# Kernel optimization log

Hardware: AMD Instinct MI355X
Metric: run time of the kernel (lower is better)

## Reference

```python
import jax, jax.numpy as jnp
import numpy as np

N = 100000      # nodes
E = 1600000     # edges (avg degree 16)
IN = 512        # input feature dim
H, C = 8, 8     # conv1: 8 heads x 8 channels (hardcoded in module)
HID = H * C     # 64
OUT = 64        # output classes (conv2: 1 head, no concat)
NEG_SLOPE = 0.2 # PyG GATConv default leaky-relu slope


def setup_inputs() -> dict:
    key = jax.random.key(0)
    ks = jax.random.split(key, 10)
    x = jax.random.normal(ks[0], (N, IN), dtype=jnp.float32)
    edge_index = jax.random.randint(ks[1], (2, E), 0, N, dtype=jnp.int32)
    W1 = jax.random.normal(ks[2], (IN, HID), dtype=jnp.float32) / np.sqrt(IN).astype(np.float32)
    a_src1 = jax.random.normal(ks[3], (H, C), dtype=jnp.float32) * 0.1
    a_dst1 = jax.random.normal(ks[4], (H, C), dtype=jnp.float32) * 0.1
    b1 = jnp.zeros((HID,), dtype=jnp.float32)
    W2 = jax.random.normal(ks[5], (HID, OUT), dtype=jnp.float32) / np.sqrt(HID).astype(np.float32)
    a_src2 = jax.random.normal(ks[6], (1, OUT), dtype=jnp.float32) * 0.1
    a_dst2 = jax.random.normal(ks[7], (1, OUT), dtype=jnp.float32) * 0.1
    b2 = jnp.zeros((OUT,), dtype=jnp.float32)
    return {"x": x, "edge_index": edge_index, "W1": W1, "a_src1": a_src1,
            "a_dst1": a_dst1, "b1": b1, "W2": W2, "a_src2": a_src2,
            "a_dst2": a_dst2, "b2": b2}


def _gat_attend(h, src, dst, a_s, a_d, n_nodes):
    """h: [N,H,C]; src/dst: [E]; a_s/a_d: [H,C] -> aggregated [N,H,C]."""
    # per-node half-scores (PyG decomposition of a^T [Wx_i || Wx_j])
    sc_s = jnp.sum(h * a_s, axis=-1)                       # [N,H]
    sc_d = jnp.sum(h * a_d, axis=-1)                       # [N,H]
    logits = jax.nn.leaky_relu(sc_s[src] + sc_d[dst], NEG_SLOPE)  # [E,H]
    # segment softmax over edges grouped by destination node
    mx = jax.ops.segment_max(logits, dst, num_segments=n_nodes)   # [N,H]
    ex = jnp.exp(logits - mx[dst])                          # [E,H]
    denom = jax.ops.segment_sum(ex, dst, num_segments=n_nodes)    # [N,H]
    alpha = ex / (denom[dst] + 1e-16)                       # [E,H]
    msg = h[src] * alpha[:, :, None]                        # [E,H,C]
    return jax.ops.segment_sum(msg, dst, num_segments=n_nodes)    # [N,H,C]


def reference(x, edge_index, W1, a_src1, a_dst1, b1, W2, a_src2, a_dst2, b2):
    n = x.shape[0]
    loop = jnp.arange(n, dtype=edge_index.dtype)
    src = jnp.concatenate([edge_index[0], loop])            # self-loops (PyG default)
    dst = jnp.concatenate([edge_index[1], loop])
    # conv1: 8 heads, concat
    h1 = (x @ W1).reshape(n, H, C)
    o1 = _gat_attend(h1, src, dst, a_src1, a_dst1, n).reshape(n, HID) + b1
    x2 = jax.nn.elu(o1)
    # conv2: 1 head, no concat
    h2 = (x2 @ W2).reshape(n, 1, OUT)
    o2 = _gat_attend(h2, src, dst, a_src2, a_dst2, n)[:, 0] + b2
    return jax.nn.log_softmax(o2, axis=1)
```

## Files before the change

kernel.cpp:

```cpp
#include <hip/hip_runtime.h>
#include <cstdint>
#include <cstddef>

#define LEAKY 0.2f
#define NEG_INF -3.402823466e38f
static const int CHUNK = 2048;

typedef __attribute__((ext_vector_type(8))) short short8;
typedef __attribute__((ext_vector_type(4))) float floatx4;

__device__ __forceinline__ float dot4(float4 a, float4 b) {
    return a.x * b.x + a.y * b.y + a.z * b.z + a.w * b.w;
}

__device__ __forceinline__ unsigned short f2bf(float f) {
    unsigned u = __float_as_uint(f);
    u += 0x7fffu + ((u >> 16) & 1u);
    return (unsigned short)(u >> 16);
}
__device__ __forceinline__ float bf2f(unsigned short u) {
    return __uint_as_float(((unsigned)u) << 16);
}
__device__ __forceinline__ float bflo(unsigned u) { return __uint_as_float(u << 16); }
__device__ __forceinline__ float bfhi(unsigned u) { return __uint_as_float(u & 0xffff0000u); }

__global__ __launch_bounds__(256) void k_init_deg(int* __restrict__ deg, int Nn) {
    int i = blockIdx.x * 256 + threadIdx.x;
    if (i < Nn) deg[i] = 1;
}

__global__ __launch_bounds__(256) void k_count_p(const int* __restrict__ ei, int* __restrict__ deg,
                                                 int E, int Nn) {
    int part = blockIdx.x & 7;
    int lo = (int)((long long)Nn * part >> 3);
    int hi = (int)((long long)Nn * (part + 1) >> 3);
    int nthr = (gridDim.x >> 3) * 256;
    int tid = (blockIdx.x >> 3) * 256 + threadIdx.x;
    for (int e = tid; e < E; e += nthr) {
        int d = ei[E + e];
        if (d >= lo && d < hi) atomicAdd(&deg[d], 1);
    }
}

__global__ __launch_bounds__(256) void k_scan1(const int* __restrict__ deg, int* __restrict__ bsum, int Nn) {
    __shared__ int sm[256];
    int b = blockIdx.x, t = threadIdx.x;
    int s = 0;
    int i0 = b * CHUNK + t * 8;
#pragma unroll
    for (int j = 0; j < 8; ++j) { int i = i0 + j; if (i < Nn) s += deg[i]; }
    sm[t] = s;
    __syncthreads();
    for (int o = 128; o; o >>= 1) { if (t < o) sm[t] += sm[t + o]; __syncthreads(); }
    if (t == 0) bsum[b] = sm[0];
}

__global__ __launch_bounds__(256) void k_scan3(const int* __restrict__ deg, const int* __restrict__ bsum,
                                               int* __restrict__ indptr, int* __restrict__ cursor,
                                               int Nn, int B) {
    __shared__ int wsum[4];
    int b = blockIdx.x, t = threadIdx.x, lane = t & 63, w = t >> 6;

    int vb = (lane < B) ? bsum[lane] : 0;
    int incb = vb;
#pragma unroll
    for (int o = 1; o < 64; o <<= 1) { int u = __shfl_up(incb, o); if (lane >= o) incb += u; }
    int bpre_b = __shfl(incb - vb, b);

    int i0 = b * CHUNK + t * 8;
    int d[8]; int s = 0;
#pragma unroll
    for (int j = 0; j < 8; ++j) { int i = i0 + j; d[j] = (i < Nn) ? deg[i] : 0; s += d[j]; }
    int inc = s;
#pragma unroll
    for (int o = 1; o < 64; o <<= 1) { int u = __shfl_up(inc, o); if (lane >= o) inc += u; }
    if (lane == 63) wsum[w] = inc;
    __syncthreads();
    int wofs = 0;
    for (int k = 0; k < w; ++k) wofs += wsum[k];
    int base = bpre_b + wofs + (inc - s);
    int run = 0;
#pragma unroll
    for (int j = 0; j < 8; ++j) {
        int i = i0 + j;
        if (i < Nn) {
            int v = base + run;
            indptr[i] = v; cursor[i] = v;
            run += d[j];
            if (i == Nn - 1) indptr[Nn] = v + d[j];
        }
    }
}

__global__ __launch_bounds__(256) void k_fill_p(const int* __restrict__ ei, int* __restrict__ cursor,
                                                int* __restrict__ csr, int E, int Nn) {
    int part = blockIdx.x & 7;
    int lo = (int)((long long)Nn * part >> 3);
    int hi = (int)((long long)Nn * (part + 1) >> 3);
    int nthr = (gridDim.x >> 3) * 256;
    int tid = (blockIdx.x >> 3) * 256 + threadIdx.x;
    int tot = E + Nn;
    for (int idx = tid; idx < tot; idx += nthr) {
        int d = (idx < E) ? ei[E + idx] : idx - E;
        if (d >= lo && d < hi) {
            int s = (idx < E) ? ei[idx] : idx - E;
            int slot = atomicAdd(&cursor[d], 1);
            csr[slot] = s;
        }
    }
}

__global__ __launch_bounds__(256) void k_prepW(const float* __restrict__ W1, unsigned short* __restrict__ W1t) {
    int i = blockIdx.x * 256 + threadIdx.x;
    if (i >= 64 * 512) return;
    int n = i >> 9, k = i & 511;
    W1t[i] = f2bf(W1[k * 64 + n]);
}

__global__ __launch_bounds__(256) void gemm1_mfma(const float* __restrict__ A, const unsigned short* __restrict__ W1t,
                                                  unsigned short* __restrict__ C, int M) {
    __shared__ __align__(16) unsigned short As[128][40];
    __shared__ __align__(16) unsigned short Bs[64][40];
    int t = threadIdx.x;
    int w = t >> 6, l = t & 63;
    int quad = l >> 4, lm = l & 15;
    int row0 = blockIdx.x * 128;

    floatx4 acc[2][4] = {};

    for (int k0 = 0; k0 < 512; k0 += 32) {
#pragma unroll
        for (int j = 0; j < 4; ++j) {
            int f = t + 256 * j;
            int r = f >> 3, c4 = f & 7;
            int rg = row0 + r; if (rg >= M) rg = M - 1;
            float4 v = *(const float4*)(A + (size_t)rg * 512 + k0 + c4 * 4);
            ushort4 b; b.x = f2bf(v.x); b.y = f2bf(v.y); b.z = f2bf(v.z); b.w = f2bf(v.w);
            *(ushort4*)&As[r][c4 * 4] = b;
        }
        {
            int n = t >> 2, seg = t & 3;
            *(uint4*)&Bs[n][seg * 8] = *(const uint4*)(W1t + (size_t)n * 512 + k0 + seg * 8);
        }
        __syncthreads();

        short8 af[2], bfm[4];
#pragma unroll
        for (int tm = 0; tm < 2; ++tm) {
            int m = w * 32 + tm * 16 + lm;
            af[tm] = *(const short8*)&As[m][quad * 8];
        }
#pragma unroll
        for (int tn = 0; tn < 4; ++tn) {
            int n = tn * 16 + lm;
            bfm[tn] = *(const short8*)&Bs[n][quad * 8];
        }
#pragma unroll
        for (int tm = 0; tm < 2; ++tm)
#pragma unroll
            for (int tn = 0; tn < 4; ++tn)
                acc[tm][tn] = __builtin_amdgcn_mfma_f32_16x16x32_bf16(af[tm], bfm[tn], acc[tm][tn], 0, 0, 0);
        __syncthreads();
    }

#pragma unroll
    for (int tm = 0; tm < 2; ++tm) {
#pragma unroll
        for (int r = 0; r < 4; ++r) {
            int row = row0 + w * 32 + tm * 16 + quad * 4 + r;
            if (row < M) {
#pragma unroll
                for (int tn = 0; tn < 4; ++tn)
                    C[(size_t)row * 64 + tn * 16 + lm] = f2bf(acc[tm][tn][r]);
            }
        }
    }
}

template <int KB>
__global__ __launch_bounds__(256) void gemm_n64(const float* __restrict__ A, const float* __restrict__ B,
                                                unsigned short* __restrict__ C, int M, int K) {
    __shared__ float As[KB][68];
    __shared__ float Bs[KB][68];
    int tid = threadIdx.x;
    int row0 = blockIdx.x * 64;
    int tx = tid & 15, ty = tid >> 4;
    float acc[4][4] = {};
    for (int k0 = 0; k0 < K; k0 += KB) {
#pragma unroll
        for (int j = 0; j < (64 * KB) / (256 * 4); ++j) {
            int f = tid + 256 * j;
            int r = f / (KB / 4);
            int c4 = f % (KB / 4);
            int rg = row0 + r; if (rg >= M) rg = M - 1;
            float4 v = *(const float4*)(A + (size_t)rg * K + k0 + c4 * 4);
            As[c4 * 4 + 0][r] = v.x; As[c4 * 4 + 1][r] = v.y;
            As[c4 * 4 + 2][r] = v.z; As[c4 * 4 + 3][r] = v.w;
        }
#pragma unroll
        for (int j = 0; j < (KB * 64) / (256 * 4); ++j) {
            int f = tid + 256 * j;
            int kk = f / 16, c4 = f % 16;
            *(float4*)&Bs[kk][c4 * 4] = *(const float4*)(B + (size_t)(k0 + kk) * 64 + c4 * 4);
        }
        __syncthreads();
#pragma unroll
        for (int kk = 0; kk < KB; ++kk) {
            float4 a = *(const float4*)&As[kk][ty * 4];
            float4 b = *(const float4*)&Bs[kk][tx * 4];
            float av[4] = {a.x, a.y, a.z, a.w};
            float bv[4] = {b.x, b.y, b.z, b.w};
#pragma unroll
            for (int i = 0; i < 4; ++i)
#pragma unroll
                for (int j = 0; j < 4; ++j) acc[i][j] += av[i] * bv[j];
        }
        __syncthreads();
    }
#pragma unroll
    for (int i = 0; i < 4; ++i) {
        int rg = row0 + ty * 4 + i;
        if (rg < M) {
            ushort4 b; b.x = f2bf(acc[i][0]); b.y = f2bf(acc[i][1]);
            b.z = f2bf(acc[i][2]); b.w = f2bf(acc[i][3]);
            *(ushort4*)(C + (size_t)rg * 64 + tx * 4) = b;
        }
    }
}

__global__ __launch_bounds__(256) void k_sc1(const unsigned short* __restrict__ h1, const float* __restrict__ as1,
                                             const float* __restrict__ ad1, float* __restrict__ scs,
                                             float* __restrict__ scd, int Nn) {
    int i = blockIdx.x * 256 + threadIdx.x;
    if (i >= Nn * 8) return;
    int h = i & 7;
    ushort4 p0 = *(const ushort4*)(h1 + (size_t)i * 8);
    ushort4 p1 = *(const ushort4*)(h1 + (size_t)i * 8 + 4);
    float4 v0 = make_float4(bf2f(p0.x), bf2f(p0.y), bf2f(p0.z), bf2f(p0.w));
    float4 v1 = make_float4(bf2f(p1.x), bf2f(p1.y), bf2f(p1.z), bf2f(p1.w));
    const float4* asp = (const float4*)(as1 + h * 8);
    const float4* adp = (const float4*)(ad1 + h * 8);
    scs[i] = dot4(v0, asp[0]) + dot4(v1, asp[1]);
    scd[i] = dot4(v0, adp[0]) + dot4(v1, adp[1]);
}

__global__ __launch_bounds__(256) void k_sc2(const unsigned short* __restrict__ h2, const float* __restrict__ as2,
                                             const float* __restrict__ ad2, float* __restrict__ scs,
                                             float* __restrict__ scd, int Nn) {
    int wave = (blockIdx.x * 256 + threadIdx.x) >> 6;
    int lane = threadIdx.x & 63;
    if (wave >= Nn) return;
    float v = bf2f(h2[(size_t)wave * 64 + lane]);
    float ss = v * as2[lane], sd = v * ad2[lane];
#pragma unroll
    for (int o = 32; o; o >>= 1) { ss += __shfl_xor(ss, o); sd += __shfl_xor(sd, o); }
    if (lane == 0) { scs[wave] = ss; scd[wave] = sd; }
}

__global__ __launch_bounds__(256) void k_agg1(const unsigned short* __restrict__ h1, const float* __restrict__ scs,
                                              const float* __restrict__ scd, const int* __restrict__ indptr,
                                              const int* __restrict__ csr, const float* __restrict__ b1,
                                              float* __restrict__ x2, int Nn) {
    int node = (blockIdx.x * 256 + threadIdx.x) >> 6;
    int l = threadIdx.x & 63;
    if (node >= Nn) return;
    int h8 = l & 7, grp = l >> 3;
    int start = indptr[node], end = indptr[node + 1];
    float sd = scd[node * 8 + h8];

    float dsum = 0.f;
    float acc8[8] = {};
    for (int base = start; base < end; base += 64) {
        int e = base + l;
        int s64 = csr[e < end ? e : start];
        int cnt = min(64, end - base);
        int nb = (cnt + 7) >> 3;
#pragma unroll
        for (int b = 0; b < 8; ++b) {
            if (b < nb) {
                int slot = base + b * 8 + grp;
                int sb = __shfl(s64, b * 8 + grp);
                float v = scs[sb * 8 + h8] + sd;
                v = v > 0.f ? v : LEAKY * v;
                float ex = (slot < end) ? __expf(v) : 0.f;
                dsum += ex;
                uint4 q = *(const uint4*)(h1 + (size_t)sb * 64 + h8 * 8);
                acc8[0] += ex * bflo(q.x); acc8[1] += ex * bfhi(q.x);
                acc8[2] += ex * bflo(q.y); acc8[3] += ex * bfhi(q.y);
                acc8[4] += ex * bflo(q.z); acc8[5] += ex * bfhi(q.z);
                acc8[6] += ex * bflo(q.w); acc8[7] += ex * bfhi(q.w);
            }
        }
    }
#pragma unroll
    for (int o = 8; o < 64; o <<= 1) {
        dsum += __shfl_xor(dsum, o);
#pragma unroll
        for (int k = 0; k < 8; ++k) acc8[k] += __shfl_xor(acc8[k], o);
    }
    if (grp == 0) {
        float inv = 1.f / (dsum + 1e-16f);
        float4 ba = *((const float4*)b1 + h8 * 2);
        float4 bb = *((const float4*)b1 + h8 * 2 + 1);
        float o0 = acc8[0] * inv + ba.x, o1 = acc8[1] * inv + ba.y;
        float o2 = acc8[2] * inv + ba.z, o3 = acc8[3] * inv + ba.w;
        float o4 = acc8[4] * inv + bb.x, o5 = acc8[5] * inv + bb.y;
        float o6 = acc8[6] * inv + bb.z, o7 = acc8[7] * inv + bb.w;
        o0 = o0 > 0.f ? o0 : expm1f(o0); o1 = o1 > 0.f ? o1 : expm1f(o1);
        o2 = o2 > 0.f ? o2 : expm1f(o2); o3 = o3 > 0.f ? o3 : expm1f(o3);
        o4 = o4 > 0.f ? o4 : expm1f(o4); o5 = o5 > 0.f ? o5 : expm1f(o5);
        o6 = o6 > 0.f ? o6 : expm1f(o6); o7 = o7 > 0.f ? o7 : expm1f(o7);
        float* dst = x2 + (size_t)node * 64 + h8 * 8;
        *(float4*)dst = make_float4(o0, o1, o2, o3);
        *(float4*)(dst + 4) = make_float4(o4, o5, o6, o7);
    }
}

__global__ __launch_bounds__(256) void k_agg2(const unsigned short* __restrict__ h2, const float* __restrict__ scs,
                                              const float* __restrict__ scd, const int* __restrict__ indptr,
                                              const int* __restrict__ csr, const float* __restrict__ b2,
                                              float* __restrict__ out, int Nn) {
    int node = (blockIdx.x * 256 + threadIdx.x) >> 6;
    int l = threadIdx.x & 63;
    if (node >= Nn) return;
    int g = l >> 3, c8 = l & 7;
    int start = indptr[node], end = indptr[node + 1];
    float sd = scd[node];

    float dsum = 0.f;
    float acc8[8] = {};
    for (int base = start; base < end; base += 64) {
        int e = base + l;
        int s64 = csr[e < end ? e : start];
        float v = scs[s64] + sd;
        v = v > 0.f ? v : LEAKY * v;
        float ex = (e < end) ? __expf(v) : 0.f;
        dsum += ex;
        int cnt = min(64, end - base);
        int nb = (cnt + 7) >> 3;
#pragma unroll 2
        for (int b = 0; b < nb; ++b) {
            float exv = __shfl(ex, b * 8 + g);
            int sb = __shfl(s64, b * 8 + g);
            uint4 q = *(const uint4*)(h2 + (size_t)sb * 64 + c8 * 8);
            acc8[0] += exv * bflo(q.x); acc8[1] += exv * bfhi(q.x);
            acc8[2] += exv * bflo(q.y); acc8[3] += exv * bfhi(q.y);
            acc8[4] += exv * bflo(q.z); acc8[5] += exv * bfhi(q.z);
            acc8[6] += exv * bflo(q.w); acc8[7] += exv * bfhi(q.w);
        }
    }
#pragma unroll
    for (int o = 32; o; o >>= 1) dsum += __shfl_xor(dsum, o);
#pragma unroll
    for (int o = 8; o < 64; o <<= 1)
#pragma unroll
        for (int k = 0; k < 8; ++k) acc8[k] += __shfl_xor(acc8[k], o);

    float inv = 1.f / (dsum + 1e-16f);
    float4 ba = *((const float4*)b2 + c8 * 2);
    float4 bb = *((const float4*)b2 + c8 * 2 + 1);
    float ov[8];
    ov[0] = acc8[0] * inv + ba.x; ov[1] = acc8[1] * inv + ba.y;
    ov[2] = acc8[2] * inv + ba.z; ov[3] = acc8[3] * inv + ba.w;
    ov[4] = acc8[4] * inv + bb.x; ov[5] = acc8[5] * inv + bb.y;
    ov[6] = acc8[6] * inv + bb.z; ov[7] = acc8[7] * inv + bb.w;

    float m2 = ov[0];
#pragma unroll
    for (int k = 1; k < 8; ++k) m2 = fmaxf(m2, ov[k]);
#pragma unroll
    for (int o = 1; o < 8; o <<= 1) m2 = fmaxf(m2, __shfl_xor(m2, o));
    float se = 0.f;
#pragma unroll
    for (int k = 0; k < 8; ++k) se += __expf(ov[k] - m2);
#pragma unroll
    for (int o = 1; o < 8; o <<= 1) se += __shfl_xor(se, o);
    float ls = m2 + __logf(se);
    if (g == 0) {
        float* dst = out + (size_t)node * 64 + c8 * 8;
        *(float4*)dst = make_float4(ov[0] - ls, ov[1] - ls, ov[2] - ls, ov[3] - ls);
        *(float4*)(dst + 4) = make_float4(ov[4] - ls, ov[5] - ls, ov[6] - ls, ov[7] - ls);
    }
}

extern "C" void kernel_launch(void* const* d_in, const int* in_sizes, int n_in,
                              void* d_out, int out_size, void* d_ws, size_t ws_size,
                              hipStream_t stream) {
    (void)n_in; (void)out_size; (void)ws_size;
    const float* x   = (const float*)d_in[0];
    const int*   ei  = (const int*)d_in[1];
    const float* W1  = (const float*)d_in[2];
    const float* as1 = (const float*)d_in[3];
    const float* ad1 = (const float*)d_in[4];
    const float* b1  = (const float*)d_in[5];
    const float* W2  = (const float*)d_in[6];
    const float* as2 = (const float*)d_in[7];
    const float* ad2 = (const float*)d_in[8];
    const float* b2  = (const float*)d_in[9];
    float* out = (float*)d_out;

    const int N = in_sizes[0] / 512;
    const int E = in_sizes[1] / 2;

    char* p = (char*)d_ws;
    auto alloc = [&](size_t bytes) -> char* {
        char* r = p; p += (bytes + 255) & ~(size_t)255; return r;
    };
    unsigned short* h1bf = (unsigned short*)alloc((size_t)N * 64 * 2);
    float* x2    = (float*)alloc((size_t)N * 64 * 4);
    unsigned short* h2bf = h1bf;
    float* sc1s  = (float*)alloc((size_t)N * 8 * 4);
    float* sc1d  = (float*)alloc((size_t)N * 8 * 4);
    float* sc2s  = (float*)alloc((size_t)N * 4);
    float* sc2d  = (float*)alloc((size_t)N * 4);
    int*   deg   = (int*)alloc((size_t)N * 4);
    int*   cursor= (int*)alloc((size_t)N * 4);
    int*   indptr= (int*)alloc((size_t)(N + 1) * 4);
    int*   csr   = (int*)alloc((size_t)(E + N) * 4);
    int*   bsum  = (int*)alloc(64 * 4);
    unsigned short* W1t = (unsigned short*)alloc(64 * 512 * 2);

    const int B = (N + CHUNK - 1) / CHUNK;

    k_init_deg<<<(N + 255) / 256, 256, 0, stream>>>(deg, N);
    k_count_p<<<1024, 256, 0, stream>>>(ei, deg, E, N);
    k_scan1  <<<B, 256, 0, stream>>>(deg, bsum, N);
    k_scan3  <<<B, 256, 0, stream>>>(deg, bsum, indptr, cursor, N, B);
    k_fill_p <<<1024, 256, 0, stream>>>(ei, cursor, csr, E, N);

    k_prepW<<<(64 * 512 + 255) / 256, 256, 0, stream>>>(W1, W1t);
    gemm1_mfma<<<(N + 127) / 128, 256, 0, stream>>>(x, W1t, h1bf, N);
    k_sc1 <<<(N * 8 + 255) / 256, 256, 0, stream>>>(h1bf, as1, ad1, sc1s, sc1d, N);
    k_agg1<<<(N + 3) / 4, 256, 0, stream>>>(h1bf, sc1s, sc1d, indptr, csr, b1, x2, N);

    gemm_n64<64><<<(N + 63) / 64, 256, 0, stream>>>(x2, W2, h2bf, N, 64);
    k_sc2 <<<(N + 3) / 4, 256, 0, stream>>>(h2bf, as2, ad2, sc2s, sc2d, N);
    k_agg2<<<(N + 3) / 4, 256, 0, stream>>>(h2bf, sc2s, sc2d, indptr, csr, b2, out, N);
}
```

Before: 629.8 us.

## Fuse attention score computation into GEMM epilogues and batch gather loads in aggregation

```diff
diff --git a/kernel.cpp b/kernel.cpp
--- a/kernel.cpp
+++ b/kernel.cpp
@@ -24,8 +24,13 @@
 __device__ __forceinline__ float bflo(unsigned u) { return __uint_as_float(u << 16); }
 __device__ __forceinline__ float bfhi(unsigned u) { return __uint_as_float(u & 0xffff0000u); }
 
-__global__ __launch_bounds__(256) void k_init_deg(int* __restrict__ deg, int Nn) {
+__global__ __launch_bounds__(256) void k_misc(const float* __restrict__ W1, unsigned short* __restrict__ W1t,
+                                              int* __restrict__ deg, int Nn) {
     int i = blockIdx.x * 256 + threadIdx.x;
+    if (i < 64 * 512) {
+        int n = i >> 9, k = i & 511;
+        W1t[i] = f2bf(W1[k * 64 + n]);
+    }
     if (i < Nn) deg[i] = 1;
 }
 
@@ -110,15 +115,10 @@
     }
 }
 
-__global__ __launch_bounds__(256) void k_prepW(const float* __restrict__ W1, unsigned short* __restrict__ W1t) {
-    int i = blockIdx.x * 256 + threadIdx.x;
-    if (i >= 64 * 512) return;
-    int n = i >> 9, k = i & 511;
-    W1t[i] = f2bf(W1[k * 64 + n]);
-}
-
 __global__ __launch_bounds__(256) void gemm1_mfma(const float* __restrict__ A, const unsigned short* __restrict__ W1t,
-                                                  unsigned short* __restrict__ C, int M) {
+                                                  unsigned short* __restrict__ C,
+                                                  const float* __restrict__ as1, const float* __restrict__ ad1,
+                                                  float* __restrict__ scs, float* __restrict__ scd, int M) {
     __shared__ __align__(16) unsigned short As[128][40];
     __shared__ __align__(16) unsigned short Bs[64][40];
     int t = threadIdx.x;
@@ -163,6 +163,11 @@
         __syncthreads();
     }
 
+    float as_l[4], ad_l[4];
+#pragma unroll
+    for (int tn = 0; tn < 4; ++tn) { as_l[tn] = as1[tn * 16 + lm]; ad_l[tn] = ad1[tn * 16 + lm]; }
+    int hbase = (l >> 3) & 1;
+
 #pragma unroll
     for (int tm = 0; tm < 2; ++tm) {
 #pragma unroll
@@ -172,6 +177,27 @@
 #pragma unroll
                 for (int tn = 0; tn < 4; ++tn)
                     C[(size_t)row * 64 + tn * 16 + lm] = f2bf(acc[tm][tn][r]);
+                float ps[4], pd[4];
+#pragma unroll
+                for (int tn = 0; tn < 4; ++tn) {
+                    ps[tn] = acc[tm][tn][r] * as_l[tn];
+                    pd[tn] = acc[tm][tn][r] * ad_l[tn];
+                }
+#pragma unroll
+                for (int o = 1; o < 8; o <<= 1) {
+#pragma unroll
+                    for (int tn = 0; tn < 4; ++tn) {
+                        ps[tn] += __shfl_xor(ps[tn], o);
+                        pd[tn] += __shfl_xor(pd[tn], o);
+                    }
+                }
+                if ((l & 7) == 0) {
+#pragma unroll
+                    for (int tn = 0; tn < 4; ++tn) {
+                        scs[(size_t)row * 8 + tn * 2 + hbase] = ps[tn];
+                        scd[(size_t)row * 8 + tn * 2 + hbase] = pd[tn];
+                    }
+                }
             }
         }
     }
@@ -179,7 +205,10 @@
 
 template <int KB>
 __global__ __launch_bounds__(256) void gemm_n64(const float* __restrict__ A, const float* __restrict__ B,
-                                                unsigned short* __restrict__ C, int M, int K) {
+                                                unsigned short* __restrict__ C,
+                                                const float* __restrict__ as2, const float* __restrict__ ad2,
+                                                float* __restrict__ sc2s, float* __restrict__ sc2d,
+                                                int M, int K) {
     __shared__ float As[KB][68];
     __shared__ float Bs[KB][68];
     int tid = threadIdx.x;
@@ -217,6 +246,9 @@
         }
         __syncthreads();
     }
+    float as_l[4], ad_l[4];
+#pragma unroll
+    for (int j = 0; j < 4; ++j) { as_l[j] = as2[tx * 4 + j]; ad_l[j] = ad2[tx * 4 + j]; }
 #pragma unroll
     for (int i = 0; i < 4; ++i) {
         int rg = row0 + ty * 4 + i;
@@ -224,43 +256,19 @@
             ushort4 b; b.x = f2bf(acc[i][0]); b.y = f2bf(acc[i][1]);
             b.z = f2bf(acc[i][2]); b.w = f2bf(acc[i][3]);
             *(ushort4*)(C + (size_t)rg * 64 + tx * 4) = b;
-        }
-    }
-}
-
-__global__ __launch_bounds__(256) void k_sc1(const unsigned short* __restrict__ h1, const float* __restrict__ as1,
-                                             const float* __restrict__ ad1, float* __restrict__ scs,
-                                             float* __restrict__ scd, int Nn) {
-    int i = blockIdx.x * 256 + threadIdx.x;
-    if (i >= Nn * 8) return;
-    int h = i & 7;
-    ushort4 p0 = *(const ushort4*)(h1 + (size_t)i * 8);
-    ushort4 p1 = *(const ushort4*)(h1 + (size_t)i * 8 + 4);
-    float4 v0 = make_float4(bf2f(p0.x), bf2f(p0.y), bf2f(p0.z), bf2f(p0.w));
-    float4 v1 = make_float4(bf2f(p1.x), bf2f(p1.y), bf2f(p1.z), bf2f(p1.w));
-    const float4* asp = (const float4*)(as1 + h * 8);
-    const float4* adp = (const float4*)(ad1 + h * 8);
-    scs[i] = dot4(v0, asp[0]) + dot4(v1, asp[1]);
-    scd[i] = dot4(v0, adp[0]) + dot4(v1, adp[1]);
-}
-
-__global__ __launch_bounds__(256) void k_sc2(const unsigned short* __restrict__ h2, const float* __restrict__ as2,
-                                             const float* __restrict__ ad2, float* __restrict__ scs,
-                                             float* __restrict__ scd, int Nn) {
-    int wave = (blockIdx.x * 256 + threadIdx.x) >> 6;
-    int lane = threadIdx.x & 63;
-    if (wave >= Nn) return;
-    float v = bf2f(h2[(size_t)wave * 64 + lane]);
-    float ss = v * as2[lane], sd = v * ad2[lane];
-#pragma unroll
-    for (int o = 32; o; o >>= 1) { ss += __shfl_xor(ss, o); sd += __shfl_xor(sd, o); }
-    if (lane == 0) { scs[wave] = ss; scd[wave] = sd; }
-}
-
-__global__ __launch_bounds__(256) void k_agg1(const unsigned short* __restrict__ h1, const float* __restrict__ scs,
-                                              const float* __restrict__ scd, const int* __restrict__ indptr,
-                                              const int* __restrict__ csr, const float* __restrict__ b1,
-                                              float* __restrict__ x2, int Nn) {
+            float ps = acc[i][0] * as_l[0] + acc[i][1] * as_l[1] + acc[i][2] * as_l[2] + acc[i][3] * as_l[3];
+            float pd = acc[i][0] * ad_l[0] + acc[i][1] * ad_l[1] + acc[i][2] * ad_l[2] + acc[i][3] * ad_l[3];
+#pragma unroll
+            for (int o = 1; o < 16; o <<= 1) { ps += __shfl_xor(ps, o); pd += __shfl_xor(pd, o); }
+            if (tx == 0) { sc2s[rg] = ps; sc2d[rg] = pd; }
+        }
+    }
+}
+
+__global__ __launch_bounds__(256, 4) void k_agg1(const unsigned short* __restrict__ h1, const float* __restrict__ scs,
+                                                 const float* __restrict__ scd, const int* __restrict__ indptr,
+                                                 const int* __restrict__ csr, const float* __restrict__ b1,
+                                                 float* __restrict__ x2, int Nn) {
     int node = (blockIdx.x * 256 + threadIdx.x) >> 6;
     int l = threadIdx.x & 63;
     if (node >= Nn) return;
@@ -275,20 +283,31 @@
         int s64 = csr[e < end ? e : start];
         int cnt = min(64, end - base);
         int nb = (cnt + 7) >> 3;
+        int sbv[8];
+#pragma unroll
+        for (int b = 0; b < 8; ++b) sbv[b] = __shfl(s64, b * 8 + grp);
+        float exv[8];
 #pragma unroll
         for (int b = 0; b < 8; ++b) {
             if (b < nb) {
-                int slot = base + b * 8 + grp;
-                int sb = __shfl(s64, b * 8 + grp);
-                float v = scs[sb * 8 + h8] + sd;
+                float v = scs[(size_t)sbv[b] * 8 + h8] + sd;
                 v = v > 0.f ? v : LEAKY * v;
-                float ex = (slot < end) ? __expf(v) : 0.f;
+                exv[b] = (base + b * 8 + grp < end) ? __expf(v) : 0.f;
+            }
+        }
+        uint4 q[8];
+#pragma unroll
+        for (int b = 0; b < 8; ++b)
+            if (b < nb) q[b] = *(const uint4*)(h1 + (size_t)sbv[b] * 64 + h8 * 8);
+#pragma unroll
+        for (int b = 0; b < 8; ++b) {
+            if (b < nb) {
+                float ex = exv[b];
                 dsum += ex;
-                uint4 q = *(const uint4*)(h1 + (size_t)sb * 64 + h8 * 8);
-                acc8[0] += ex * bflo(q.x); acc8[1] += ex * bfhi(q.x);
-                acc8[2] += ex * bflo(q.y); acc8[3] += ex * bfhi(q.y);
-                acc8[4] += ex * bflo(q.z); acc8[5] += ex * bfhi(q.z);
-                acc8[6] += ex * bflo(q.w); acc8[7] += ex * bfhi(q.w);
+                acc8[0] += ex * bflo(q[b].x); acc8[1] += ex * bfhi(q[b].x);
+                acc8[2] += ex * bflo(q[b].y); acc8[3] += ex * bfhi(q[b].y);
+                acc8[4] += ex * bflo(q[b].z); acc8[5] += ex * bfhi(q[b].z);
+                acc8[6] += ex * bflo(q[b].w); acc8[7] += ex * bfhi(q[b].w);
             }
         }
     }
@@ -316,10 +335,10 @@
     }
 }
 
-__global__ __launch_bounds__(256) void k_agg2(const unsigned short* __restrict__ h2, const float* __restrict__ scs,
-                                              const float* __restrict__ scd, const int* __restrict__ indptr,
-                                              const int* __restrict__ csr, const float* __restrict__ b2,
-                                              float* __restrict__ out, int Nn) {
+__global__ __launch_bounds__(256, 4) void k_agg2(const unsigned short* __restrict__ h2, const float* __restrict__ scs,
+                                                 const float* __restrict__ scd, const int* __restrict__ indptr,
+                                                 const int* __restrict__ csr, const float* __restrict__ b2,
+                                                 float* __restrict__ out, int Nn) {
     int node = (blockIdx.x * 256 + threadIdx.x) >> 6;
     int l = threadIdx.x & 63;
     if (node >= Nn) return;
@@ -338,15 +357,25 @@
         dsum += ex;
         int cnt = min(64, end - base);
         int nb = (cnt + 7) >> 3;
-#pragma unroll 2
-        for (int b = 0; b < nb; ++b) {
-            float exv = __shfl(ex, b * 8 + g);
-            int sb = __shfl(s64, b * 8 + g);
-            uint4 q = *(const uint4*)(h2 + (size_t)sb * 64 + c8 * 8);
-            acc8[0] += exv * bflo(q.x); acc8[1] += exv * bfhi(q.x);
-            acc8[2] += exv * bflo(q.y); acc8[3] += exv * bfhi(q.y);
-            acc8[4] += exv * bflo(q.z); acc8[5] += exv * bfhi(q.z);
-            acc8[6] += exv * bflo(q.w); acc8[7] += exv * bfhi(q.w);
+        float exv[8]; int sbv[8];
+#pragma unroll
+        for (int b = 0; b < 8; ++b) {
+            exv[b] = __shfl(ex, b * 8 + g);
+            sbv[b] = __shfl(s64, b * 8 + g);
+        }
+        uint4 q[8];
+#pragma unroll
+        for (int b = 0; b < 8; ++b)
+            if (b < nb) q[b] = *(const uint4*)(h2 + (size_t)sbv[b] * 64 + c8 * 8);
+#pragma unroll
+        for (int b = 0; b < 8; ++b) {
+            if (b < nb) {
+                float exq = exv[b];
+                acc8[0] += exq * bflo(q[b].x); acc8[1] += exq * bfhi(q[b].x);
+                acc8[2] += exq * bflo(q[b].y); acc8[3] += exq * bfhi(q[b].y);
+                acc8[4] += exq * bflo(q[b].z); acc8[5] += exq * bfhi(q[b].z);
+                acc8[6] += exq * bflo(q[b].w); acc8[7] += exq * bfhi(q[b].w);
+            }
         }
     }
 #pragma unroll
@@ -422,18 +451,17 @@
 
     const int B = (N + CHUNK - 1) / CHUNK;
 
-    k_init_deg<<<(N + 255) / 256, 256, 0, stream>>>(deg, N);
+    const int miscGrid = (((64 * 512) > N ? (64 * 512) : N) + 255) / 256;
+    k_misc<<<miscGrid, 256, 0, stream>>>(W1, W1t, deg, N);
+
     k_count_p<<<1024, 256, 0, stream>>>(ei, deg, E, N);
     k_scan1  <<<B, 256, 0, stream>>>(deg, bsum, N);
     k_scan3  <<<B, 256, 0, stream>>>(deg, bsum, indptr, cursor, N, B);
     k_fill_p <<<1024, 256, 0, stream>>>(ei, cursor, csr, E, N);
 
-    k_prepW<<<(64 * 512 + 255) / 256, 256, 0, stream>>>(W1, W1t);
-    gemm1_mfma<<<(N + 127) / 128, 256, 0, stream>>>(x, W1t, h1bf, N);
-    k_sc1 <<<(N * 8 + 255) / 256, 256, 0, stream>>>(h1bf, as1, ad1, sc1s, sc1d, N);
+    gemm1_mfma<<<(N + 127) / 128, 256, 0, stream>>>(x, W1t, h1bf, as1, ad1, sc1s, sc1d, N);
     k_agg1<<<(N + 3) / 4, 256, 0, stream>>>(h1bf, sc1s, sc1d, indptr, csr, b1, x2, N);
 
-    gemm_n64<64><<<(N + 63) / 64, 256, 0, stream>>>(x2, W2, h2bf, N, 64);
-    k_sc2 <<<(N + 3) / 4, 256, 0, stream>>>(h2bf, as2, ad2, sc2s, sc2d, N);
+    gemm_n64<64><<<(N + 63) / 64, 256, 0, stream>>>(x2, W2, h2bf, as2, ad2, sc2s, sc2d, N, 64);
     k_agg2<<<(N + 3) / 4, 256, 0, stream>>>(h2bf, sc2s, sc2d, indptr, csr, b2, out, N);
 }
```

Result: slower. 649.8 us (+3.2%).
